# Kernel optimization log

Hardware: AMD Instinct MI355X
Metric: run time of the kernel (lower is better)

Reference implementation:

```python
import jax, jax.numpy as jnp
import numpy as np

HEADS, DH, RS = 8, 32, 16  # heads, dim_head, reduce_size

def _dwconv(x, w):
    # depthwise 3x3, pad=1, stride=1 (OIHW with I=1, groups=C)
    return jax.lax.conv_general_dilated(x, w, (1, 1), [(1, 1), (1, 1)],
        dimension_numbers=('NCHW', 'OIHW', 'NCHW'), feature_group_count=x.shape[1])

def _pwconv(x, w):
    return jax.lax.conv_general_dilated(x, w, (1, 1), 'VALID',
        dimension_numbers=('NCHW', 'OIHW', 'NCHW'))

def _bilinear_ac(x, oh, ow):
    # F.interpolate(mode='bilinear', align_corners=True)
    B, C, H, W = x.shape
    ys = jnp.linspace(0., H - 1., oh)
    xs = jnp.linspace(0., W - 1., ow)
    y0 = jnp.floor(ys).astype(jnp.int32); y1 = jnp.minimum(y0 + 1, H - 1)
    x0 = jnp.floor(xs).astype(jnp.int32); x1 = jnp.minimum(x0 + 1, W - 1)
    wy = (ys - y0)[None, None, :, None]
    wx = (xs - x0)[None, None, None, :]
    top = x[:, :, y0, :] * (1. - wy) + x[:, :, y1, :] * wy
    return top[:, :, :, x0] * (1. - wx) + top[:, :, :, x1] * wx

def _ln(t, g, b, eps=1e-6):
    # per-head LayerNorm over last dim; g,b: [heads, dim_head]
    mu = t.mean(-1, keepdims=True)
    var = ((t - mu) ** 2).mean(-1, keepdims=True)
    return (t - mu) / jnp.sqrt(var + eps) * g[None, :, None, :] + b[None, :, None, :]

def setup_inputs() -> dict:
    key = jax.random.key(0)
    ks = jax.random.split(key, 6)
    C = HEADS * DH  # 256
    x = jax.random.normal(ks[0], (8, C, 64, 64), jnp.float32)
    qkv_dw = jax.random.normal(ks[1], (C, 1, 3, 3), jnp.float32) * 0.05
    qkv_pw = jax.random.normal(ks[2], (3 * C, C, 1, 1), jnp.float32) * 0.05
    out_dw = jax.random.normal(ks[3], (C, 1, 3, 3), jnp.float32) * 0.05
    out_pw = jax.random.normal(ks[4], (C, C, 1, 1), jnp.float32) * 0.05
    gq = jnp.ones((HEADS, DH), jnp.float32); bq = jnp.zeros((HEADS, DH), jnp.float32)
    gk = jnp.ones((HEADS, DH), jnp.float32); bk = jnp.zeros((HEADS, DH), jnp.float32)
    bias_table = jax.random.normal(ks[5], ((2 * RS - 1) * (2 * RS - 1), HEADS), jnp.float32) * 0.02
    # relative_position_index buffer, exactly as in RelativePositionBias.__init__
    coords = np.stack(np.meshgrid(np.arange(RS), np.arange(RS), indexing='ij')).reshape(2, -1)
    rel = (coords[:, :, None] - coords[:, None, :]).transpose(1, 2, 0).copy()
    rel[:, :, 0] += RS - 1; rel[:, :, 1] += RS - 1; rel[:, :, 0] *= 2 * RS - 1
    rel_index = jnp.asarray(rel.sum(-1), jnp.int32)  # [RS*RS, RS*RS]
    return dict(x=x, qkv_dw=qkv_dw, qkv_pw=qkv_pw, out_dw=out_dw, out_pw=out_pw,
                gq=gq, bq=bq, gk=gk, bk=bk, bias_table=bias_table, rel_index=rel_index)

def reference(x, qkv_dw, qkv_pw, out_dw, out_pw, gq, bq, gk, bk, bias_table, rel_index):
    B, C, H, W = x.shape
    qkv = _pwconv(_dwconv(x, qkv_dw), qkv_pw)          # [B, 3*inner_dim, H, W]
    q, k, v = jnp.split(qkv, 3, axis=1)
    k = _bilinear_ac(k, RS, RS)
    v = _bilinear_ac(v, RS, RS)
    def heads(t):  # 'b (dim_head heads) h w -> b heads (h w) dim_head'
        b, _, hh, ww = t.shape
        return t.reshape(b, DH, HEADS, hh * ww).transpose(0, 2, 3, 1)
    q = _ln(heads(q), gq, bq)                           # [B, h, H*W, DH]
    k = _ln(heads(k), gk, bk)                           # [B, h, RS*RS, DH]
    v = heads(v)
    attn = jnp.einsum('bhid,bhjd->bhij', q, k)          # [B, h, H*W, RS*RS]
    # relative position bias: gather + repeat_interleave expansion
    bias = bias_table[rel_index.reshape(-1)].reshape(RS, RS, RS * RS, HEADS)
    bias = jnp.repeat(jnp.repeat(bias, H // RS, axis=0), W // RS, axis=1)
    bias = bias.reshape(H * W, RS * RS, HEADS).transpose(2, 0, 1)[None]
    attn = (attn + bias) * (1.0 / DH)                   # scale = dim_head ** -1 (no softmax)
    out = jnp.einsum('bhij,bhjd->bhid', attn, v)        # [B, h, H*W, DH]
    out = out.reshape(B, HEADS, H, W, DH).transpose(0, 4, 1, 2, 3).reshape(B, DH * HEADS, H, W)
    out = _pwconv(_dwconv(out, out_dw), out_pw)
    return out, attn
```

## Files before the change

kernel.cpp:

```cpp
#include <hip/hip_runtime.h>
#include <cstdint>

#define HW_ 4096

typedef __attribute__((ext_vector_type(8))) short bf16x8;
typedef __attribute__((ext_vector_type(4))) short bf16x4;
typedef __attribute__((ext_vector_type(4))) float f32x4;

static __device__ __forceinline__ unsigned short f2bf(float f) {
  unsigned u = __builtin_bit_cast(unsigned, f);
  u += 0x7FFF + ((u >> 16) & 1);
  return (unsigned short)(u >> 16);
}
static __device__ __forceinline__ float bf2f(unsigned short u) {
  return __builtin_bit_cast(float, (unsigned)u << 16);
}
static __device__ __forceinline__ float ldf(const float* p) { return *p; }
static __device__ __forceinline__ float ldf(const unsigned short* p) { return bf2f(*p); }

static __device__ __forceinline__ void gl_lds16(const unsigned short* g,
                                                unsigned short* s) {
  __builtin_amdgcn_global_load_lds(
      (const __attribute__((address_space(1))) unsigned int*)g,
      (__attribute__((address_space(3))) unsigned int*)s, 16, 0, 0);
}

template <typename T, int DO_PREP>
__global__ __launch_bounds__(256) void dwconv_t_kernel(
    const T* __restrict__ x, const float* __restrict__ w9,
    unsigned short* __restrict__ xT,
    const float* __restrict__ pw1, const float* __restrict__ pw2,
    unsigned short* __restrict__ wb, const float* __restrict__ btab,
    const int* __restrict__ relidx, float* __restrict__ bias_pre) {
  if (DO_PREP && blockIdx.z == 8) {
    int idx0 = (blockIdx.y * 64 + blockIdx.x) * 256 + threadIdx.x;
#pragma unroll
    for (int k = 0; k < 12; ++k) {
      int idx = idx0 + k * 65536;
      if (idx < 262144) {
        wb[idx] = f2bf(idx < 196608 ? pw1[idx] : pw2[idx - 196608]);
      } else {
        int t = idx - 262144;
        int j = t & 255, g = (t >> 8) & 255, h = t >> 16;
        bias_pre[t] = btab[relidx[g * 256 + j] * 8 + h] * 0.03125f;
      }
    }
    return;
  }
  __shared__ unsigned short lds_t[64][66];
  int iy = blockIdx.x;
  int cg = blockIdx.y;
  int b  = blockIdx.z;
  int tid = threadIdx.x;
  int px  = tid & 63;
  int cl0 = (tid >> 6) * 16;
  const T* xrow = x + (size_t)b * 256 * HW_ + iy * 64 + px;
#pragma unroll 4
  for (int e = 0; e < 16; ++e) {
    int c = cg * 64 + cl0 + e;
    const T* xp = xrow + (size_t)c * HW_;
    const float* wp = w9 + c * 9;
    float v0 = (iy > 0)  ? ldf(xp - 64) : 0.f;
    float v1 = ldf(xp);
    float v2 = (iy < 63) ? ldf(xp + 64) : 0.f;
    float l0 = __shfl(v0, px - 1, 64), r0 = __shfl(v0, px + 1, 64);
    float l1 = __shfl(v1, px - 1, 64), r1 = __shfl(v1, px + 1, 64);
    float l2 = __shfl(v2, px - 1, 64), r2 = __shfl(v2, px + 1, 64);
    if (px == 0)  { l0 = 0.f; l1 = 0.f; l2 = 0.f; }
    if (px == 63) { r0 = 0.f; r1 = 0.f; r2 = 0.f; }
    float acc = l0 * wp[0] + v0 * wp[1] + r0 * wp[2]
              + l1 * wp[3] + v1 * wp[4] + r1 * wp[5]
              + l2 * wp[6] + v2 * wp[7] + r2 * wp[8];
    lds_t[cl0 + e][px] = f2bf(acc);
  }
  __syncthreads();
#pragma unroll
  for (int j = 0; j < 2; ++j) {
    int flat = tid + j * 256;
    int rpx = flat >> 3, cseg = flat & 7;
    unsigned v0 = (unsigned)lds_t[cseg*8+0][rpx] | ((unsigned)lds_t[cseg*8+1][rpx] << 16);
    unsigned v1 = (unsigned)lds_t[cseg*8+2][rpx] | ((unsigned)lds_t[cseg*8+3][rpx] << 16);
    unsigned v2 = (unsigned)lds_t[cseg*8+4][rpx] | ((unsigned)lds_t[cseg*8+5][rpx] << 16);
    unsigned v3 = (unsigned)lds_t[cseg*8+6][rpx] | ((unsigned)lds_t[cseg*8+7][rpx] << 16);
    uint4 pk = {v0, v1, v2, v3};
    *(uint4*)(xT + ((size_t)b * 4096 + iy * 64 + rpx) * 256 + cg * 64 + cseg * 8) = pk;
  }
}

template <int OUT_BF16>
__global__ __launch_bounds__(256) void pwconv_mfma_kernel(
    const unsigned short* __restrict__ XT, const unsigned short* __restrict__ W,
    void* __restrict__ Yv, int OC) {
  __shared__ unsigned short As[128 * 64];
  __shared__ unsigned short Bs[128 * 64];
  int b = blockIdx.z, oc0 = blockIdx.y * 128, p0 = blockIdx.x * 128;
  int tid = threadIdx.x;
  int w = tid >> 6, l = tid & 63;
  int wm = w >> 1, wn = w & 1;
  int lr = l & 15, lg = l >> 4;
  const unsigned short* Wp = W + (size_t)oc0 * 256;
  const unsigned short* Xp = XT + ((size_t)b * 4096 + p0) * 256;
  f32x4 acc[4][4] = {};
  for (int kt = 0; kt < 4; ++kt) {
    int k0 = kt * 64;
#pragma unroll
    for (int j = 0; j < 4; ++j) {
      int chunk = w * 4 + j;
      int row = chunk * 8 + (l >> 3);
      int lcu = (l & 7) ^ (row & 7);
      gl_lds16(Wp + (size_t)row * 256 + k0 + lcu * 8, &As[chunk * 512]);
      gl_lds16(Xp + (size_t)row * 256 + k0 + lcu * 8, &Bs[chunk * 512]);
    }
    __syncthreads();
#pragma unroll
    for (int ks = 0; ks < 2; ++ks) {
      bf16x8 af[4], bfr[4];
      int ku = ks * 4 + lg;
#pragma unroll
      for (int mi = 0; mi < 4; ++mi) {
        int row = wm * 64 + mi * 16 + lr;
        af[mi] = *(const bf16x8*)&As[row * 64 + (ku ^ (row & 7)) * 8];
      }
#pragma unroll
      for (int ni = 0; ni < 4; ++ni) {
        int row = wn * 64 + ni * 16 + lr;
        bfr[ni] = *(const bf16x8*)&Bs[row * 64 + (ku ^ (row & 7)) * 8];
      }
#pragma unroll
      for (int mi = 0; mi < 4; ++mi)
#pragma unroll
        for (int ni = 0; ni < 4; ++ni)
          acc[mi][ni] = __builtin_amdgcn_mfma_f32_16x16x32_bf16(
              af[mi], bfr[ni], acc[mi][ni], 0, 0, 0);
    }
    __syncthreads();
  }
  if constexpr (OUT_BF16) {
    __shared__ unsigned short Cs[128][136];
#pragma unroll
    for (int mi = 0; mi < 4; ++mi)
#pragma unroll
      for (int ni = 0; ni < 4; ++ni)
#pragma unroll
        for (int r = 0; r < 4; ++r)
          Cs[wm * 64 + mi * 16 + lg * 4 + r][wn * 64 + ni * 16 + lr] =
              f2bf(acc[mi][ni][r]);
    __syncthreads();
    unsigned short* Yb = (unsigned short*)Yv + (size_t)b * OC * HW_;
    int pc = tid & 15, ocr = tid >> 4;
#pragma unroll
    for (int it = 0; it < 8; ++it) {
      int oc = it * 16 + ocr;
      uint4 pk = *(const uint4*)&Cs[oc][pc * 8];
      *(uint4*)(Yb + (size_t)(oc0 + oc) * HW_ + p0 + pc * 8) = pk;
    }
  } else {
    float* Yb = (float*)Yv + (size_t)b * OC * HW_;
#pragma unroll
    for (int mi = 0; mi < 4; ++mi)
#pragma unroll
      for (int ni = 0; ni < 4; ++ni)
#pragma unroll
        for (int r = 0; r < 4; ++r) {
          int oc = oc0 + wm * 64 + mi * 16 + lg * 4 + r;
          int p  = p0 + wn * 64 + ni * 16 + lr;
          Yb[(size_t)oc * HW_ + p] = acc[mi][ni][r];
        }
  }
}

__global__ __launch_bounds__(256) void bilin_kvln_kernel(
    const unsigned short* __restrict__ qkvb, const float* __restrict__ g,
    const float* __restrict__ bb, unsigned short* __restrict__ kln,
    unsigned short* __restrict__ vfrag) {
  int bx = blockIdx.x;
  int bh = bx >> 2, jt = bx & 3;
  int h = bh & 7, b = bh >> 3;
  int tid = threadIdx.x;
  int jloc = tid >> 2, dg = tid & 3;
  int j = jt * 64 + jloc;
  int oy = j >> 4, ox = j & 15;
  const float s = 63.0f / 15.0f;
  float ys = oy * s, xf = ox * s;
  int y0 = (int)ys, x0 = (int)xf;
  int y1 = min(y0 + 1, 63), x1 = min(x0 + 1, 63);
  float wy = ys - (float)y0, wx = xf - (float)x0;
  float kv[8], vv[8];
  float sum = 0.f, sum2 = 0.f;
#pragma unroll
  for (int e = 0; e < 8; ++e) {
    int d = dg * 8 + e;
    const unsigned short* kp = qkvb + ((size_t)b * 768 + 256 + d * 8 + h) * HW_;
    const unsigned short* vp = qkvb + ((size_t)b * 768 + 512 + d * 8 + h) * HW_;
    float k00 = bf2f(kp[y0*64+x0]), k01 = bf2f(kp[y0*64+x1]);
    float k10 = bf2f(kp[y1*64+x0]), k11 = bf2f(kp[y1*64+x1]);
    float ktop = k00 * (1.f - wx) + k01 * wx;
    float kbot = k10 * (1.f - wx) + k11 * wx;
    kv[e] = ktop * (1.f - wy) + kbot * wy;
    float v00 = bf2f(vp[y0*64+x0]), v01 = bf2f(vp[y0*64+x1]);
    float v10 = bf2f(vp[y1*64+x0]), v11 = bf2f(vp[y1*64+x1]);
    float vtop = v00 * (1.f - wx) + v01 * wx;
    float vbot = v10 * (1.f - wx) + v11 * wx;
    vv[e] = vtop * (1.f - wy) + vbot * wy;
    sum += kv[e]; sum2 += kv[e] * kv[e];
  }
  sum  += __shfl_xor(sum, 1, 64);  sum  += __shfl_xor(sum, 2, 64);
  sum2 += __shfl_xor(sum2, 1, 64); sum2 += __shfl_xor(sum2, 2, 64);
  float mu = sum * (1.f / 32.f);
  float var = sum2 * (1.f / 32.f) - mu * mu;
  float inv = 1.0f / sqrtf(var + 1e-6f);
  unsigned r[4];
#pragma unroll
  for (int t = 0; t < 4; ++t) {
    int d0 = dg * 8 + 2 * t;
    float y0f = (kv[2*t]   - mu) * inv * g[h*32 + d0]     + bb[h*32 + d0];
    float y1f = (kv[2*t+1] - mu) * inv * g[h*32 + d0 + 1] + bb[h*32 + d0 + 1];
    r[t] = (unsigned)f2bf(y0f) | ((unsigned)f2bf(y1f) << 16);
  }
  uint4 pk = {r[0], r[1], r[2], r[3]};
  *(uint4*)(kln + ((size_t)bh * 256 + j) * 32 + dg * 8) = pk;
  int c = j >> 4, gq = (j >> 2) & 3, ii = j & 3;
  unsigned short* vo = vfrag + (size_t)bh * 32 * 256;
#pragma unroll
  for (int e = 0; e < 8; ++e) {
    int d = dg * 8 + e;
    int dt = d >> 4, dr = d & 15;
    vo[(c * 2 + dt) * 256 + (gq * 16 + dr) * 4 + ii] = f2bf(vv[e]);
  }
}

__global__ __launch_bounds__(256) void attn_mfma_kernel(
    const unsigned short* __restrict__ qkvb, const float* __restrict__ gq,
    const float* __restrict__ bq, const unsigned short* __restrict__ kln,
    const unsigned short* __restrict__ vfrag, const float* __restrict__ bias_pre,
    float* __restrict__ attn_out, unsigned short* __restrict__ out_nchw) {
  int tile = blockIdx.x, h = blockIdx.y, b = blockIdx.z;
  int bh = b * 8 + h;
  int tid = threadIdx.x;
  int w = tid >> 6, l = tid & 63;
  int lr = l & 15, lg = l >> 4;
  int qbase = tile * 64 + w * 16;
  int q = qbase + lr;
  int iy = q >> 6, ix = q & 63;
  int g = (iy >> 2) * 16 + (ix >> 2);

  const unsigned short* qp = qkvb + ((size_t)b * 768 + h) * HW_ + q;
  float qv[8];
  float sum = 0.f, sum2 = 0.f;
#pragma unroll
  for (int e = 0; e < 8; ++e) {
    qv[e] = bf2f(qp[(size_t)((lg * 8 + e) * 8) * HW_]);
    sum += qv[e]; sum2 += qv[e] * qv[e];
  }
  sum  += __shfl_xor(sum, 16, 64);  sum  += __shfl_xor(sum, 32, 64);
  sum2 += __shfl_xor(sum2, 16, 64); sum2 += __shfl_xor(sum2, 32, 64);
  float mu = sum * (1.f / 32.f);
  float var = sum2 * (1.f / 32.f) - mu * mu;
  float inv = 1.0f / sqrtf(var + 1e-6f);
  bf16x8 qf;
#pragma unroll
  for (int e = 0; e < 8; ++e) {
    int d = lg * 8 + e;
    float y = (qv[e] - mu) * inv * gq[h * 32 + d] + bq[h * 32 + d];
    qf[e] = (short)f2bf(y);
  }

  const unsigned short* kbase = kln + (size_t)bh * 256 * 32 + lr * 32 + lg * 8;
  const unsigned short* vbase = vfrag + (size_t)bh * 32 * 256 + l * 4;
  const float* bbase = bias_pre + ((size_t)h * 256 + g) * 256 + lg * 4;
  float* abase = attn_out + ((size_t)bh * 4096 + q) * 256 + lg * 4;

  f32x4 z = {0.f, 0.f, 0.f, 0.f};
  f32x4 oacc0 = z, oacc1 = z;
#pragma unroll
  for (int c = 0; c < 16; ++c) {
    bf16x8 kf = *(const bf16x8*)(kbase + c * 16 * 32);
    f32x4 s = __builtin_amdgcn_mfma_f32_16x16x32_bf16(kf, qf, z, 0, 0, 0);
    f32x4 bias = *(const f32x4*)(bbase + c * 16);
    f32x4 t = s * 0.03125f + bias;
    __builtin_nontemporal_store(t, (f32x4*)(abase + c * 16));
    bf16x4 pb;
    pb[0] = (short)f2bf(t.x);
    pb[1] = (short)f2bf(t.y);
    pb[2] = (short)f2bf(t.z);
    pb[3] = (short)f2bf(t.w);
    bf16x4 va0 = *(const bf16x4*)(vbase + (c * 2 + 0) * 256);
    bf16x4 va1 = *(const bf16x4*)(vbase + (c * 2 + 1) * 256);
    oacc0 = __builtin_amdgcn_mfma_f32_16x16x16bf16_1k(va0, pb, oacc0, 0, 0, 0);
    oacc1 = __builtin_amdgcn_mfma_f32_16x16x16bf16_1k(va1, pb, oacc1, 0, 0, 0);
  }
  float ov[8] = {oacc0.x, oacc0.y, oacc0.z, oacc0.w,
                 oacc1.x, oacc1.y, oacc1.z, oacc1.w};
#pragma unroll
  for (int dt = 0; dt < 2; ++dt) {
#pragma unroll
    for (int r = 0; r < 4; ++r) {
      int d = dt * 16 + lg * 4 + r;
      int cc = d * 8 + h;
      out_nchw[((size_t)b * 256 + cc) * HW_ + qbase + lr] = f2bf(ov[dt * 4 + r]);
    }
  }
}

extern "C" void kernel_launch(void* const* d_in, const int* in_sizes, int n_in,
                              void* d_out, int out_size, void* d_ws, size_t ws_size,
                              hipStream_t stream) {
  const float* x      = (const float*)d_in[0];
  const float* qkv_dw = (const float*)d_in[1];
  const float* qkv_pw = (const float*)d_in[2];
  const float* out_dw = (const float*)d_in[3];
  const float* out_pw = (const float*)d_in[4];
  const float* gq     = (const float*)d_in[5];
  const float* bq     = (const float*)d_in[6];
  const float* gk     = (const float*)d_in[7];
  const float* bk     = (const float*)d_in[8];
  const float* btab   = (const float*)d_in[9];
  const int*   relidx = (const int*)d_in[10];

  float* out  = (float*)d_out;
  float* attn = out + 8388608;

  unsigned short* us = (unsigned short*)d_ws;
  unsigned short* xT1    = us;
  unsigned short* xT2    = us + 8388608;
  unsigned short* onchwb = us + 16777216;
  unsigned short* kln    = us + 25165824;
  unsigned short* vfrag  = us + 25690112;
  unsigned short* wbuf   = us + 26214400;
  float* bias_pre = (float*)(us + 26476544);
  unsigned short* qkvb   = us + 27525120;

  dwconv_t_kernel<float, 1><<<dim3(64, 4, 9), 256, 0, stream>>>(
      x, qkv_dw, xT1, qkv_pw, out_pw, wbuf, btab, relidx, bias_pre);
  pwconv_mfma_kernel<1><<<dim3(32, 6, 8), 256, 0, stream>>>(xT1, wbuf, qkvb, 768);
  bilin_kvln_kernel<<<256, 256, 0, stream>>>(qkvb, gk, bk, kln, vfrag);
  attn_mfma_kernel<<<dim3(64, 8, 8), 256, 0, stream>>>(qkvb, gq, bq, kln, vfrag,
                                                       bias_pre, attn, onchwb);
  dwconv_t_kernel<unsigned short, 0><<<dim3(64, 4, 8), 256, 0, stream>>>(
      onchwb, out_dw, xT2, nullptr, nullptr, nullptr, nullptr, nullptr, nullptr);
  pwconv_mfma_kernel<0><<<dim3(32, 2, 8), 256, 0, stream>>>(xT2, wbuf + 196608, out, 256);
}
```

Baseline: 154.4 us.

## Bilinear-downsample before K/V projection and fuse K/V LayerNorm into pwconv

The pointwise conv and bilinear resize are both linear, so they commute. The code now resizes the depthwise-conv output to 16x16 first and only then projects to K and V, inside an extra blockIdx.y slice of the pwconv kernel. That slice also applies the K LayerNorm and writes the V fragment layout. This drops the full-resolution K/V projection (two thirds of the first GEMM's output), the qkv K/V round trip through memory, and the separate bilinear/LN kernel launch. In exchange, the K/V path uses scalar FMA rather than MFMA, and bf16 rounding now happens at different points.

```diff
diff --git a/kernel.cpp b/kernel.cpp
--- a/kernel.cpp
+++ b/kernel.cpp
@@ -87,14 +87,93 @@
   }
 }
 
-template <int OUT_BF16>
+template <int OUT_BF16, int KV>
 __global__ __launch_bounds__(256) void pwconv_mfma_kernel(
     const unsigned short* __restrict__ XT, const unsigned short* __restrict__ W,
-    void* __restrict__ Yv, int OC) {
+    void* __restrict__ Yv, int OC,
+    const float* __restrict__ gk, const float* __restrict__ bk,
+    unsigned short* __restrict__ kln, unsigned short* __restrict__ vfrag) {
   __shared__ unsigned short As[128 * 64];
   __shared__ unsigned short Bs[128 * 64];
-  int b = blockIdx.z, oc0 = blockIdx.y * 128, p0 = blockIdx.x * 128;
   int tid = threadIdx.x;
+  int b = blockIdx.z;
+  if (KV && blockIdx.y == 2) {
+    float (*xds)[260] = (float(*)[260])As;
+    int j0 = blockIdx.x * 8;
+    {
+      int pt = tid >> 5, icg = tid & 31;
+      int j = j0 + pt;
+      int oy = j >> 4, ox = j & 15;
+      const float s = 63.0f / 15.0f;
+      float ys = oy * s, xf = ox * s;
+      int y0 = (int)ys, x0 = (int)xf;
+      int y1 = min(y0 + 1, 63), x1 = min(x0 + 1, 63);
+      float wy = ys - (float)y0, wx = xf - (float)x0;
+      float w00 = (1.f - wy) * (1.f - wx), w01 = (1.f - wy) * wx;
+      float w10 = wy * (1.f - wx), w11 = wy * wx;
+      const unsigned short* base = XT + (size_t)b * 4096 * 256 + icg * 8;
+      bf16x8 a00 = *(const bf16x8*)(base + (size_t)(y0 * 64 + x0) * 256);
+      bf16x8 a01 = *(const bf16x8*)(base + (size_t)(y0 * 64 + x1) * 256);
+      bf16x8 a10 = *(const bf16x8*)(base + (size_t)(y1 * 64 + x0) * 256);
+      bf16x8 a11 = *(const bf16x8*)(base + (size_t)(y1 * 64 + x1) * 256);
+#pragma unroll
+      for (int e = 0; e < 8; ++e) {
+        xds[pt][icg * 8 + e] =
+            w00 * bf2f((unsigned short)a00[e]) + w01 * bf2f((unsigned short)a01[e]) +
+            w10 * bf2f((unsigned short)a10[e]) + w11 * bf2f((unsigned short)a11[e]);
+      }
+    }
+    __syncthreads();
+    int pt = tid & 7, grp = tid >> 3;
+    int isv = grp >> 4, h = (grp >> 1) & 7, dh = grp & 1;
+    int j = j0 + pt;
+    int bh = b * 8 + h;
+    float acc[16] = {};
+    const unsigned short* Wb = W + (size_t)(256 + isv * 256 + dh * 128 + h) * 256;
+    for (int c8 = 0; c8 < 32; ++c8) {
+      const float4* xr = (const float4*)&xds[pt][c8 * 8];
+      float4 xa = xr[0], xb = xr[1];
+#pragma unroll
+      for (int dd = 0; dd < 16; ++dd) {
+        bf16x8 wv = *(const bf16x8*)(Wb + (size_t)dd * 8 * 256 + c8 * 8);
+        acc[dd] += bf2f((unsigned short)wv[0]) * xa.x + bf2f((unsigned short)wv[1]) * xa.y
+                 + bf2f((unsigned short)wv[2]) * xa.z + bf2f((unsigned short)wv[3]) * xa.w
+                 + bf2f((unsigned short)wv[4]) * xb.x + bf2f((unsigned short)wv[5]) * xb.y
+                 + bf2f((unsigned short)wv[6]) * xb.z + bf2f((unsigned short)wv[7]) * xb.w;
+      }
+    }
+    if (isv == 0) {
+      float s1 = 0.f, s2 = 0.f;
+#pragma unroll
+      for (int dd = 0; dd < 16; ++dd) { s1 += acc[dd]; s2 += acc[dd] * acc[dd]; }
+      s1 += __shfl_xor(s1, 8, 64);
+      s2 += __shfl_xor(s2, 8, 64);
+      float mu = s1 * (1.f / 32.f);
+      float var = s2 * (1.f / 32.f) - mu * mu;
+      float inv = 1.0f / sqrtf(var + 1e-6f);
+      unsigned r[8];
+#pragma unroll
+      for (int t = 0; t < 8; ++t) {
+        int d = dh * 16 + 2 * t;
+        float y0f = (acc[2*t]   - mu) * inv * gk[h*32 + d]     + bk[h*32 + d];
+        float y1f = (acc[2*t+1] - mu) * inv * gk[h*32 + d + 1] + bk[h*32 + d + 1];
+        r[t] = (unsigned)f2bf(y0f) | ((unsigned)f2bf(y1f) << 16);
+      }
+      unsigned short* ko = kln + ((size_t)bh * 256 + j) * 32 + dh * 16;
+      uint4 p0 = {r[0], r[1], r[2], r[3]};
+      uint4 p1 = {r[4], r[5], r[6], r[7]};
+      *(uint4*)ko = p0;
+      *(uint4*)(ko + 8) = p1;
+    } else {
+      int c = j >> 4, gq2 = (j >> 2) & 3, ii = j & 3;
+      unsigned short* vo = vfrag + (size_t)bh * 32 * 256 + (c * 2 + dh) * 256 + ii;
+#pragma unroll
+      for (int dd = 0; dd < 16; ++dd)
+        vo[(gq2 * 16 + dd) * 4] = f2bf(acc[dd]);
+    }
+    return;
+  }
+  int oc0 = blockIdx.y * 128, p0 = blockIdx.x * 128;
   int w = tid >> 6, l = tid & 63;
   int wm = w >> 1, wn = w & 1;
   int lr = l & 15, lg = l >> 4;
@@ -169,68 +248,8 @@
   }
 }
 
-__global__ __launch_bounds__(256) void bilin_kvln_kernel(
-    const unsigned short* __restrict__ qkvb, const float* __restrict__ g,
-    const float* __restrict__ bb, unsigned short* __restrict__ kln,
-    unsigned short* __restrict__ vfrag) {
-  int bx = blockIdx.x;
-  int bh = bx >> 2, jt = bx & 3;
-  int h = bh & 7, b = bh >> 3;
-  int tid = threadIdx.x;
-  int jloc = tid >> 2, dg = tid & 3;
-  int j = jt * 64 + jloc;
-  int oy = j >> 4, ox = j & 15;
-  const float s = 63.0f / 15.0f;
-  float ys = oy * s, xf = ox * s;
-  int y0 = (int)ys, x0 = (int)xf;
-  int y1 = min(y0 + 1, 63), x1 = min(x0 + 1, 63);
-  float wy = ys - (float)y0, wx = xf - (float)x0;
-  float kv[8], vv[8];
-  float sum = 0.f, sum2 = 0.f;
-#pragma unroll
-  for (int e = 0; e < 8; ++e) {
-    int d = dg * 8 + e;
-    const unsigned short* kp = qkvb + ((size_t)b * 768 + 256 + d * 8 + h) * HW_;
-    const unsigned short* vp = qkvb + ((size_t)b * 768 + 512 + d * 8 + h) * HW_;
-    float k00 = bf2f(kp[y0*64+x0]), k01 = bf2f(kp[y0*64+x1]);
-    float k10 = bf2f(kp[y1*64+x0]), k11 = bf2f(kp[y1*64+x1]);
-    float ktop = k00 * (1.f - wx) + k01 * wx;
-    float kbot = k10 * (1.f - wx) + k11 * wx;
-    kv[e] = ktop * (1.f - wy) + kbot * wy;
-    float v00 = bf2f(vp[y0*64+x0]), v01 = bf2f(vp[y0*64+x1]);
-    float v10 = bf2f(vp[y1*64+x0]), v11 = bf2f(vp[y1*64+x1]);
-    float vtop = v00 * (1.f - wx) + v01 * wx;
-    float vbot = v10 * (1.f - wx) + v11 * wx;
-    vv[e] = vtop * (1.f - wy) + vbot * wy;
-    sum += kv[e]; sum2 += kv[e] * kv[e];
-  }
-  sum  += __shfl_xor(sum, 1, 64);  sum  += __shfl_xor(sum, 2, 64);
-  sum2 += __shfl_xor(sum2, 1, 64); sum2 += __shfl_xor(sum2, 2, 64);
-  float mu = sum * (1.f / 32.f);
-  float var = sum2 * (1.f / 32.f) - mu * mu;
-  float inv = 1.0f / sqrtf(var + 1e-6f);
-  unsigned r[4];
-#pragma unroll
-  for (int t = 0; t < 4; ++t) {
-    int d0 = dg * 8 + 2 * t;
-    float y0f = (kv[2*t]   - mu) * inv * g[h*32 + d0]     + bb[h*32 + d0];
-    float y1f = (kv[2*t+1] - mu) * inv * g[h*32 + d0 + 1] + bb[h*32 + d0 + 1];
-    r[t] = (unsigned)f2bf(y0f) | ((unsigned)f2bf(y1f) << 16);
-  }
-  uint4 pk = {r[0], r[1], r[2], r[3]};
-  *(uint4*)(kln + ((size_t)bh * 256 + j) * 32 + dg * 8) = pk;
-  int c = j >> 4, gq = (j >> 2) & 3, ii = j & 3;
-  unsigned short* vo = vfrag + (size_t)bh * 32 * 256;
-#pragma unroll
-  for (int e = 0; e < 8; ++e) {
-    int d = dg * 8 + e;
-    int dt = d >> 4, dr = d & 15;
-    vo[(c * 2 + dt) * 256 + (gq * 16 + dr) * 4 + ii] = f2bf(vv[e]);
-  }
-}
-
 __global__ __launch_bounds__(256) void attn_mfma_kernel(
-    const unsigned short* __restrict__ qkvb, const float* __restrict__ gq,
+    const unsigned short* __restrict__ qb, const float* __restrict__ gq,
     const float* __restrict__ bq, const unsigned short* __restrict__ kln,
     const unsigned short* __restrict__ vfrag, const float* __restrict__ bias_pre,
     float* __restrict__ attn_out, unsigned short* __restrict__ out_nchw) {
@@ -244,7 +263,7 @@
   int iy = q >> 6, ix = q & 63;
   int g = (iy >> 2) * 16 + (ix >> 2);
 
-  const unsigned short* qp = qkvb + ((size_t)b * 768 + h) * HW_ + q;
+  const unsigned short* qp = qb + ((size_t)b * 256 + h) * HW_ + q;
   float qv[8];
   float sum = 0.f, sum2 = 0.f;
 #pragma unroll
@@ -328,15 +347,16 @@
   unsigned short* vfrag  = us + 25690112;
   unsigned short* wbuf   = us + 26214400;
   float* bias_pre = (float*)(us + 26476544);
-  unsigned short* qkvb   = us + 27525120;
+  unsigned short* qb     = us + 27525120;
 
   dwconv_t_kernel<float, 1><<<dim3(64, 4, 9), 256, 0, stream>>>(
       x, qkv_dw, xT1, qkv_pw, out_pw, wbuf, btab, relidx, bias_pre);
-  pwconv_mfma_kernel<1><<<dim3(32, 6, 8), 256, 0, stream>>>(xT1, wbuf, qkvb, 768);
-  bilin_kvln_kernel<<<256, 256, 0, stream>>>(qkvb, gk, bk, kln, vfrag);
-  attn_mfma_kernel<<<dim3(64, 8, 8), 256, 0, stream>>>(qkvb, gq, bq, kln, vfrag,
+  pwconv_mfma_kernel<1, 1><<<dim3(32, 3, 8), 256, 0, stream>>>(
+      xT1, wbuf, qb, 256, gk, bk, kln, vfrag);
+  attn_mfma_kernel<<<dim3(64, 8, 8), 256, 0, stream>>>(qb, gq, bq, kln, vfrag,
                                                        bias_pre, attn, onchwb);
   dwconv_t_kernel<unsigned short, 0><<<dim3(64, 4, 8), 256, 0, stream>>>(
       onchwb, out_dw, xT2, nullptr, nullptr, nullptr, nullptr, nullptr, nullptr);
-  pwconv_mfma_kernel<0><<<dim3(32, 2, 8), 256, 0, stream>>>(xT2, wbuf + 196608, out, 256);
-}
+  pwconv_mfma_kernel<0, 0><<<dim3(32, 2, 8), 256, 0, stream>>>(
+      xT2, wbuf + 196608, out, 256, nullptr, nullptr, nullptr, nullptr);
+}
```

Measured after the change: 168.6 us. 9.2% more time.
